# Performance work log

Measured on AMD Instinct MI355X. Metric: run time of the kernel, lower is better.

Reference implementation:

```python
import jax, jax.numpy as jnp
import numpy as np

BN_EPS = 1e-5


def _lin(x, W, b):
    return x @ W.T + b


def reference(input, first_skeleton, noise, first_W, first_b, gru_Wih, gru_Whh,
              gru_bih, gru_bhh, l0_W, l0_b, res_W, res_b, bn_g, bn_b, bn_m, bn_v,
              fl1_W, fl1_b, fl2_W, fl2_b, fl3_W, fl3_b, qkv_W,
              posm_W1, posm_b1, posm_W2, posm_b2, attn_W1, attn_b1, attn_W2, attn_b2):
    B = input.shape[0]
    # first skeleton embedding -> (B, 50, 1)
    sk = _lin(first_skeleton.reshape(B, 36), first_W, first_b).reshape(B, 50, 1)
    # GRU(10 -> 10), batch_first, h0 = 0
    def gru_step(h, x_t):
        gi = x_t @ gru_Wih.T + gru_bih          # (B, 30)
        gh = h @ gru_Whh.T + gru_bhh
        ir, iz, i_n = jnp.split(gi, 3, axis=-1)
        hr, hz, h_n = jnp.split(gh, 3, axis=-1)
        r = jax.nn.sigmoid(ir + hr)
        z = jax.nn.sigmoid(iz + hz)
        n = jnp.tanh(i_n + r * h_n)
        h_new = (1.0 - z) * n + z * h
        return h_new, h_new
    h0 = jnp.zeros((B, 10), input.dtype)
    _, aux = jax.lax.scan(gru_step, h0, jnp.swapaxes(noise, 0, 1))  # (50, B, 10)
    aux = jnp.tanh(jnp.swapaxes(aux, 0, 1))                          # (B, 50, 10)
    x = jnp.concatenate([input, aux, sk], axis=2).reshape(-1, 267)   # (B*50, 267)
    out = _lin(x, l0_W, l0_b)                                        # (B*50, 1024)
    # three residual Linear+BN(eval)+ReLU blocks
    for i in range(3):
        y = out
        for j in range(2):
            y = _lin(y, res_W[i, j], res_b[i, j])
            y = bn_g[i, j] * (y - bn_m[i, j]) * jax.lax.rsqrt(bn_v[i, j] + BN_EPS) + bn_b[i, j]
            y = jax.nn.relu(y)
        out = y + out
    # dropout: eval mode (identity)
    feats = _lin(out, fl1_W, fl1_b).reshape(B, 50, 128)
    pos = _lin(out, fl2_W, fl2_b).reshape(B, 50, 3)
    # PointTransformerLayer (full attention, mask all True -> no-op)
    qkv = feats @ qkv_W.T                                   # (B, 50, 384)
    q, k, v = jnp.split(qkv, 3, axis=-1)
    rel_pos = pos[:, :, None, :] - pos[:, None, :, :]        # (B, 50, 50, 3)
    rel_emb = _lin(jax.nn.relu(_lin(rel_pos, posm_W1, posm_b1)), posm_W2, posm_b2)  # (B,50,50,128)
    qk_rel = q[:, :, None, :] - k[:, None, :, :]             # (B, 50, 50, 128)
    v_ij = v[:, None, :, :] + rel_emb                        # (B, 50, 50, 128)
    sim = _lin(jax.nn.relu(_lin(qk_rel + rel_emb, attn_W1, attn_b1)), attn_W2, attn_b2)
    attn = jax.nn.softmax(sim, axis=-2)                      # softmax over j
    agg = jnp.einsum('bijd,bijd->bid', attn, v_ij)           # (B, 50, 128)
    o = jnp.tanh(_lin(agg, fl3_W, fl3_b))                    # (B, 50, 36)
    return o


def setup_inputs() -> dict:
    key = jax.random.key(0)
    ks = iter(jax.random.split(key, 64))
    def W(*s):
        return jax.random.normal(next(ks), s, jnp.float32) * 0.02
    B = 256
    z = lambda *s: jnp.zeros(s, jnp.float32)
    return {
        'input': jax.random.normal(next(ks), (B, 50, 256), jnp.float32),
        'first_skeleton': jax.random.normal(next(ks), (B, 36), jnp.float32),
        'noise': jax.random.normal(next(ks), (B, 50, 10), jnp.float32) * 0.33,
        'first_W': W(50, 36), 'first_b': z(50),
        'gru_Wih': W(30, 10), 'gru_Whh': W(30, 10), 'gru_bih': z(30), 'gru_bhh': z(30),
        'l0_W': W(1024, 267), 'l0_b': z(1024),
        'res_W': W(3, 2, 1024, 1024), 'res_b': z(3, 2, 1024),
        'bn_g': jnp.ones((3, 2, 1024), jnp.float32), 'bn_b': z(3, 2, 1024),
        'bn_m': z(3, 2, 1024), 'bn_v': jnp.ones((3, 2, 1024), jnp.float32),
        'fl1_W': W(128, 1024), 'fl1_b': z(128),
        'fl2_W': W(3, 1024), 'fl2_b': z(3),
        'fl3_W': W(36, 128), 'fl3_b': z(36),
        'qkv_W': W(384, 128),
        'posm_W1': W(64, 3), 'posm_b1': z(64), 'posm_W2': W(128, 64), 'posm_b2': z(128),
        'attn_W1': W(512, 128), 'attn_b1': z(512), 'attn_W2': W(128, 512), 'attn_b2': z(128),
    }
```

## Files before the change

kernel.cpp:

```cpp
#include <hip/hip_runtime.h>

typedef __attribute__((ext_vector_type(8))) short bf16x8;
typedef __attribute__((ext_vector_type(4))) float f32x4;
typedef __attribute__((ext_vector_type(4))) ushort u16x4;

__device__ __forceinline__ unsigned f2b2(float lo, float hi) {
    unsigned r;
    asm("v_cvt_pk_bf16_f32 %0, %1, %2" : "=v"(r) : "v"(lo), "v"(hi));
    return r;
}
__device__ __forceinline__ ushort f2b(float v) {
    return (ushort)f2b2(v, v);
}
__device__ __forceinline__ float b2f(ushort b) {
    union { float f; unsigned u; } x; x.u = ((unsigned)b) << 16; return x.f;
}

__device__ __forceinline__ void gl_lds16(const void* g, void* l) {
    __builtin_amdgcn_global_load_lds(
        (__attribute__((address_space(1))) void*)(g),
        (__attribute__((address_space(3))) void*)(l), 16, 0, 0);
}


__global__ void k_split(const float* __restrict__ src, ushort* __restrict__ hi,
                        ushort* __restrict__ lo, int rows, int K, int Kpad) {
    long total = (long)rows * Kpad;
    for (long idx = (long)blockIdx.x * 256 + threadIdx.x; idx < total;
         idx += (long)gridDim.x * 256) {
        int r = (int)(idx / Kpad), c = (int)(idx % Kpad);
        float v = (c < K) ? src[(long)r * K + c] : 0.f;
        ushort h = f2b(v);
        hi[idx] = h;
        if (lo) lo[idx] = f2b(v - b2f(h));
    }
}

__global__ void k_wc(const float* __restrict__ qkvW, const float* __restrict__ fl1W,
                     const float* __restrict__ fl1b, float* __restrict__ Wc,
                     float* __restrict__ bc) {
    int idx = blockIdx.x * 256 + threadIdx.x;
    if (idx >= 384 * 1024) return;
    int n = idx >> 10, k = idx & 1023;
    float s = 0.f;
    #pragma unroll 8
    for (int d = 0; d < 128; ++d) s += qkvW[n * 128 + d] * fl1W[d * 1024 + k];
    Wc[idx] = s;
    if (k == 0) {
        float sb = 0.f;
        #pragma unroll 8
        for (int d = 0; d < 128; ++d) sb += qkvW[n * 128 + d] * fl1b[d];
        bc[n] = sb;
    }
}

__global__ void k_sk(const float* __restrict__ fs, const float* __restrict__ fW,
                     const float* __restrict__ fb, float* __restrict__ sk) {
    int m = blockIdx.x * 256 + threadIdx.x;
    if (m >= 12800) return;
    int b = m / 50, i = m % 50;
    float s = fb[i];
    #pragma unroll 4
    for (int c = 0; c < 36; ++c) s += fs[b * 36 + c] * fW[i * 36 + c];
    sk[m] = s;
}

__global__ void k_gru(const float* __restrict__ noise, const float* __restrict__ Wih,
                      const float* __restrict__ Whh, const float* __restrict__ bih,
                      const float* __restrict__ bhh, float* __restrict__ aux) {
    int lane = threadIdx.x & 63;
    int b = blockIdx.x;
    if (b >= 256) return;
    float wih[10] = {}, whh[10] = {};
    float bi = 0.f, bh = 0.f;
    if (lane < 30) {
        #pragma unroll
        for (int c = 0; c < 10; ++c) { wih[c] = Wih[lane * 10 + c]; whh[c] = Whh[lane * 10 + c]; }
        bi = bih[lane]; bh = bhh[lane];
    }
    float h = 0.f;
    for (int t = 0; t < 50; ++t) {
        float xr = (lane < 10) ? noise[(b * 50 + t) * 10 + lane] : 0.f;
        float gi = bi, gh = bh;
        #pragma unroll
        for (int c = 0; c < 10; ++c) {
            float xc = __shfl(xr, c, 64);
            float hc = __shfl(h, c, 64);
            gi += wih[c] * xc; gh += whh[c] * hc;
        }
        float siz = __shfl(gi, lane + 10, 64), shz = __shfl(gh, lane + 10, 64);
        float sin_ = __shfl(gi, lane + 20, 64), shn = __shfl(gh, lane + 20, 64);
        float r = 1.f / (1.f + expf(-(gi + gh)));
        float z = 1.f / (1.f + expf(-(siz + shz)));
        float n = tanhf(sin_ + r * shn);
        float hn = (1.f - z) * n + z * h;
        if (lane < 10) { h = hn; aux[(b * 50 + t) * 10 + lane] = tanhf(hn); }
    }
}

__global__ void k_xbuild(const float* __restrict__ input, const float* __restrict__ aux,
                         const float* __restrict__ sk, ushort* __restrict__ xhi,
                         long M) {
    long idx = (long)blockIdx.x * 256 + threadIdx.x;
    if (idx >= M * 288) return;
    int m = (int)(idx / 288), c = (int)(idx % 288);
    float v;
    if (c < 256) v = input[(long)m * 256 + c];
    else if (c < 266) v = aux[m * 10 + (c - 256)];
    else if (c == 266) v = sk[m];
    else v = 0.f;
    xhi[idx] = f2b(v);
}

template <int MODE>
__global__ __launch_bounds__(256, 3) void k_gemm(
    const ushort* __restrict__ Ahi,
    const ushort* __restrict__ Bhi,
    int N, int K,
    float* outF, ushort* outHi,
    const float* __restrict__ bias,
    const float* __restrict__ bng, const float* __restrict__ bnb,
    const float* __restrict__ bnm, const float* __restrict__ bnv,
    const ushort* resHi) {
    __shared__ __align__(16) ushort S[2][128][32];
    int t = threadIdx.x;
    int flat = blockIdx.y * gridDim.x + blockIdx.x;
    int nwg = gridDim.x * gridDim.y;
    int q = nwg >> 3, r = nwg & 7;
    int xcd = flat & 7, seq = flat >> 3;
    int wgid = (xcd < r ? xcd * (q + 1) : r * (q + 1) + (xcd - r) * q) + seq;
    int bx = wgid % gridDim.x, by = wgid / gridDim.x;
    int m0 = by * 128, n0 = bx * 128;
    int w = t >> 6, lane = t & 63;
    int wm = w >> 1, wn = w & 1;
    int lo16 = lane & 15, hi4 = lane >> 4;

    const int srow = lane >> 2;
    const int skoff = ((lane & 3) ^ (srow & 3)) * 8;
    const int slot8 = (hi4 ^ (lo16 & 3)) * 8;

    f32x4 acc[4][4];
    #pragma unroll
    for (int i = 0; i < 4; ++i)
        #pragma unroll
        for (int j = 0; j < 4; ++j) acc[i][j] = f32x4{0.f, 0.f, 0.f, 0.f};

    const int nk = K / 32;
    for (int kt = 0; kt < nk; ++kt) {
        const int kb = kt * 32;
        #pragma unroll
        for (int i = 0; i < 2; ++i) {
            int rg = w * 32 + i * 16;
            long ga = (long)(m0 + rg + srow) * K + kb + skoff;
            long gb = (long)(n0 + rg + srow) * K + kb + skoff;
            gl_lds16(&Ahi[ga], &S[0][rg][0]);
            gl_lds16(&Bhi[gb], &S[1][rg][0]);
        }
        __syncthreads();
        bf16x8 ah[4], bh[4];
        #pragma unroll
        for (int m = 0; m < 4; ++m) {
            int row = wm * 64 + m * 16 + lo16;
            ah[m] = *(const bf16x8*)&S[0][row][slot8];
        }
        #pragma unroll
        for (int n = 0; n < 4; ++n) {
            int col = wn * 64 + n * 16 + lo16;
            bh[n] = *(const bf16x8*)&S[1][col][slot8];
        }
        #pragma unroll
        for (int m = 0; m < 4; ++m)
            #pragma unroll
            for (int n = 0; n < 4; ++n)
                acc[m][n] = __builtin_amdgcn_mfma_f32_16x16x32_bf16(ah[m], bh[n], acc[m][n], 0, 0, 0);
        __syncthreads();
    }

    #pragma unroll
    for (int n = 0; n < 4; ++n) {
        int gn = n0 + wn * 64 + n * 16 + lo16;
        float bv = bias ? bias[gn] : 0.f;
        float sc = 1.f, sh = 0.f;
        if (MODE >= 1) { sc = bng[gn] * rsqrtf(bnv[gn] + 1e-5f); sh = bnb[gn] - bnm[gn] * sc; }
        #pragma unroll
        for (int m = 0; m < 4; ++m)
            #pragma unroll
            for (int r2 = 0; r2 < 4; ++r2) {
                int gm = m0 + wm * 64 + m * 16 + hi4 * 4 + r2;
                long o = (long)gm * N + gn;
                float v = acc[m][n][r2] + bv;
                if (MODE >= 1) v = fmaxf(v * sc + sh, 0.f);
                if (MODE == 2) v += b2f(resHi[o]);
                if (outF) outF[o] = v;
                if (outHi) outHi[o] = f2b(v);
            }
    }
}

__global__ void k_fl2(const ushort* __restrict__ hA,
                      const float* __restrict__ W, const float* __restrict__ bias,
                      float* __restrict__ pos) {
    int w = threadIdx.x >> 6, lane = threadIdx.x & 63;
    int m = blockIdx.x * 4 + w;
    float a0 = 0.f, a1 = 0.f, a2 = 0.f;
    for (int k0 = lane * 4; k0 < 1024; k0 += 256) {
        long o = (long)m * 1024 + k0;
        u16x4 hv = *(const u16x4*)&hA[o];
        f32x4 w0 = *(const f32x4*)&W[k0];
        f32x4 w1 = *(const f32x4*)&W[1024 + k0];
        f32x4 w2 = *(const f32x4*)&W[2048 + k0];
        #pragma unroll
        for (int e = 0; e < 4; ++e) {
            float x = b2f(hv[e]);
            a0 += x * w0[e]; a1 += x * w1[e]; a2 += x * w2[e];
        }
    }
    #pragma unroll
    for (int off = 32; off; off >>= 1) {
        a0 += __shfl_xor(a0, off, 64);
        a1 += __shfl_xor(a1, off, 64);
        a2 += __shfl_xor(a2, off, 64);
    }
    if (lane == 0) {
        pos[m * 3 + 0] = a0 + bias[0];
        pos[m * 3 + 1] = a1 + bias[1];
        pos[m * 3 + 2] = a2 + bias[2];
    }
}

__global__ __launch_bounds__(256, 3) void k_sim(
    const float* __restrict__ qkv, const float* __restrict__ posb,
    const ushort* __restrict__ W1b, const ushort* __restrict__ W2b,
    const float* __restrict__ b1, const ushort* __restrict__ pW2b,
    const float* __restrict__ pW1, const float* __restrict__ pb1,
    const float* __restrict__ pb2, _Float16* __restrict__ sim) {
    __shared__ __align__(16) char smem[49152];
    int flat = blockIdx.x;
    int nwg = gridDim.x;
    int q = nwg >> 3, r = nwg & 7;
    int xcd = flat & 7, seq = flat >> 3;
    int wgid = (xcd < r ? xcd * (q + 1) : r * (q + 1) + (xcd - r) * q) + seq;
    int R0 = wgid * 128;
    int t = threadIdx.x, w = t >> 6, lane = t & 63;
    int lo16 = lane & 15, hi4 = lane >> 4;
    char* H1 = smem + 32768;

    {
        int rl = t & 127, eh = t >> 7;
        int g = R0 + rl;
        int bi = g / 50, j = g - bi * 50;
        int b = bi / 50;
        int kv = b * 50 + j;
        float d0 = posb[bi * 3] - posb[kv * 3];
        float d1 = posb[bi * 3 + 1] - posb[kv * 3 + 1];
        float d2 = posb[bi * 3 + 2] - posb[kv * 3 + 2];
        int swm = (rl & 7) << 4;
        #pragma unroll
        for (int e0 = 0; e0 < 32; e0 += 2) {
            int e = eh * 32 + e0;
            float v0 = fmaxf(pb1[e] + pW1[e * 3] * d0 + pW1[e * 3 + 1] * d1
                             + pW1[e * 3 + 2] * d2, 0.f);
            float v1 = fmaxf(pb1[e + 1] + pW1[e * 3 + 3] * d0 + pW1[e * 3 + 4] * d1
                             + pW1[e * 3 + 5] * d2, 0.f);
            *(unsigned*)(H1 + rl * 128 + ((e * 2) ^ swm)) = f2b2(v0, v1);
        }
    }
    __syncthreads();

    {
        f32x4 racc[8][2];
        #pragma unroll
        for (int m = 0; m < 8; ++m)
            #pragma unroll
            for (int n = 0; n < 2; ++n) racc[m][n] = f32x4{0.f, 0.f, 0.f, 0.f};
        #pragma unroll
        for (int kt = 0; kt < 2; ++kt) {
            int k0 = kt * 32 + hi4 * 8;
            bf16x8 bv[2];
            #pragma unroll
            for (int n = 0; n < 2; ++n)
                bv[n] = *(const bf16x8*)&pW2b[(w * 32 + n * 16 + lo16) * 64 + k0];
            #pragma unroll
            for (int m = 0; m < 8; ++m) {
                int row = m * 16 + lo16;
                bf16x8 ha = *(const bf16x8*)(H1 + row * 128 + ((k0 * 2) ^ ((lo16 & 7) << 4)));
                #pragma unroll
                for (int n = 0; n < 2; ++n)
                    racc[m][n] = __builtin_amdgcn_mfma_f32_16x16x32_bf16(ha, bv[n], racc[m][n], 0, 0, 0);
            }
        }
        #pragma unroll
        for (int m = 0; m < 8; ++m)
            #pragma unroll
            for (int n = 0; n < 2; ++n) {
                int col = w * 32 + n * 16 + lo16;
                float pb = pb2[col];
                #pragma unroll
                for (int rr = 0; rr < 4; ++rr) {
                    int row = m * 16 + hi4 * 4 + rr;
                    *(ushort*)(smem + row * 256 + ((col * 2) ^ ((row & 15) << 4))) =
                        f2b(racc[m][n][rr] + pb);
                }
            }
    }
    __syncthreads();

    #pragma unroll
    for (int cc = 0; cc < 8; ++cc) {
        int c = cc * 256 + t;
        int row = c >> 4, g16 = c & 15;
        int g = R0 + row;
        int bi = g / 50, j = g - bi * 50;
        int b = bi / 50;
        long kq = (long)bi * 384 + g16 * 8;
        long kk = (long)(b * 50 + j) * 384 + 128 + g16 * 8;
        f32x4 q0 = *(const f32x4*)&qkv[kq];
        f32x4 q1 = *(const f32x4*)&qkv[kq + 4];
        f32x4 k0v = *(const f32x4*)&qkv[kk];
        f32x4 k1v = *(const f32x4*)&qkv[kk + 4];
        char* addr = smem + row * 256 + ((g16 * 16) ^ ((row & 15) << 4));
        bf16x8 rv = *(bf16x8*)addr;
        bf16x8 tv;
        unsigned* tu = (unsigned*)&tv;
        #pragma unroll
        for (int i = 0; i < 2; ++i)
            tu[i] = f2b2(q0[2 * i] - k0v[2 * i] + b2f((ushort)rv[2 * i]),
                         q0[2 * i + 1] - k0v[2 * i + 1] + b2f((ushort)rv[2 * i + 1]));
        #pragma unroll
        for (int i = 0; i < 2; ++i)
            tu[2 + i] = f2b2(q1[2 * i] - k1v[2 * i] + b2f((ushort)rv[4 + 2 * i]),
                             q1[2 * i + 1] - k1v[2 * i + 1] + b2f((ushort)rv[4 + 2 * i + 1]));
        *(bf16x8*)addr = tv;
    }
    __syncthreads();

    f32x4 acc2[8][2];
    #pragma unroll
    for (int m = 0; m < 8; ++m)
        #pragma unroll
        for (int n = 0; n < 2; ++n) acc2[m][n] = f32x4{0.f, 0.f, 0.f, 0.f};

    for (int e8 = 0; e8 < 8; ++e8) {
        f32x4 acc1[8];
        #pragma unroll
        for (int m = 0; m < 8; ++m) acc1[m] = f32x4{0.f, 0.f, 0.f, 0.f};
        __builtin_amdgcn_s_setprio(1);
        #pragma unroll
        for (int kt = 0; kt < 4; ++kt) {
            int col = e8 * 64 + w * 16 + lo16;
            int k0 = kt * 32 + hi4 * 8;
            bf16x8 bfv = *(const bf16x8*)&W1b[(long)col * 128 + k0];
            #pragma unroll
            for (int m = 0; m < 8; ++m) {
                int row = m * 16 + lo16;
                bf16x8 af = *(const bf16x8*)(smem + row * 256 +
                              ((k0 * 2) ^ ((row & 15) << 4)));
                acc1[m] = __builtin_amdgcn_mfma_f32_16x16x32_bf16(af, bfv, acc1[m], 0, 0, 0);
            }
        }
        __builtin_amdgcn_s_setprio(0);
        __syncthreads();
        {
            int ch = w * 16 + lo16;
            float bb = b1[e8 * 64 + ch];
            #pragma unroll
            for (int m = 0; m < 8; ++m) {
                unsigned p01 = f2b2(fmaxf(acc1[m][0] + bb, 0.f), fmaxf(acc1[m][1] + bb, 0.f));
                unsigned p23 = f2b2(fmaxf(acc1[m][2] + bb, 0.f), fmaxf(acc1[m][3] + bb, 0.f));
                int r0 = m * 16 + hi4 * 4;
                *(ushort*)(H1 + (r0 + 0) * 128 + ((ch * 2) ^ (((r0 + 0) & 7) << 4))) = (ushort)p01;
                *(ushort*)(H1 + (r0 + 1) * 128 + ((ch * 2) ^ (((r0 + 1) & 7) << 4))) = (ushort)(p01 >> 16);
                *(ushort*)(H1 + (r0 + 2) * 128 + ((ch * 2) ^ (((r0 + 2) & 7) << 4))) = (ushort)p23;
                *(ushort*)(H1 + (r0 + 3) * 128 + ((ch * 2) ^ (((r0 + 3) & 7) << 4))) = (ushort)(p23 >> 16);
            }
        }
        __syncthreads();
        #pragma unroll
        for (int kt2 = 0; kt2 < 2; ++kt2) {
            int k0 = kt2 * 32 + hi4 * 8;
            bf16x8 af2[8];
            #pragma unroll
            for (int m = 0; m < 8; ++m) {
                int row = m * 16 + lo16;
                af2[m] = *(const bf16x8*)(H1 + row * 128 + ((k0 * 2) ^ ((lo16 & 7) << 4)));
            }
            __builtin_amdgcn_s_setprio(1);
            #pragma unroll
            for (int n = 0; n < 2; ++n) {
                int col = w * 32 + n * 16 + lo16;
                bf16x8 w2 = *(const bf16x8*)&W2b[(long)col * 512 + e8 * 64 + k0];
                #pragma unroll
                for (int m = 0; m < 8; ++m)
                    acc2[m][n] = __builtin_amdgcn_mfma_f32_16x16x32_bf16(af2[m], w2, acc2[m][n], 0, 0, 0);
            }
            __builtin_amdgcn_s_setprio(0);
        }
    }

    #pragma unroll
    for (int m = 0; m < 8; ++m)
        #pragma unroll
        for (int n = 0; n < 2; ++n) {
            int col = w * 32 + n * 16 + lo16;
            #pragma unroll
            for (int rr = 0; rr < 4; ++rr) {
                int row = m * 16 + hi4 * 4 + rr;
                sim[(long)(R0 + row) * 128 + col] = (_Float16)acc2[m][n][rr];
            }
        }
}

__global__ __launch_bounds__(256, 3) void k_soft(
    const float* __restrict__ qkv, const float* __restrict__ posb,
    const ushort* __restrict__ pW2b,
    const float* __restrict__ pW1, const float* __restrict__ pb1,
    const float* __restrict__ pb2, const _Float16* __restrict__ sim,
    const float* __restrict__ fl3W, const float* __restrict__ fl3b,
    float* __restrict__ out, long mbase) {
    __shared__ __align__(16) char smem[17472];
    int cpx = gridDim.x >> 3;
    int biL = (blockIdx.x & 7) * cpx + (blockIdx.x >> 3);
    int bL = biL / 50;
    int t = threadIdx.x, w = t >> 6, lane = t & 63;
    int lo16 = lane & 15, hi4 = lane >> 4;

    bf16x8 h_a[2];
    {
        const int jrow = w * 16 + lo16;
        const bool jvalid = jrow < 50;
        float pi0 = posb[biL * 3], pi1 = posb[biL * 3 + 1], pi2 = posb[biL * 3 + 2];
        float d0 = 0.f, d1 = 0.f, d2 = 0.f;
        if (jvalid) {
            int pj = (bL * 50 + jrow) * 3;
            d0 = pi0 - posb[pj]; d1 = pi1 - posb[pj + 1]; d2 = pi2 - posb[pj + 2];
        }
        #pragma unroll
        for (int kt = 0; kt < 2; ++kt) {
            float hv[8];
            #pragma unroll
            for (int e = 0; e < 8; ++e) {
                int ke = kt * 32 + hi4 * 8 + e;
                hv[e] = jvalid
                    ? fmaxf(pb1[ke] + pW1[ke * 3] * d0 + pW1[ke * 3 + 1] * d1
                            + pW1[ke * 3 + 2] * d2, 0.f)
                    : 0.f;
            }
            unsigned* hu = (unsigned*)&h_a[kt];
            #pragma unroll
            for (int i = 0; i < 4; ++i) hu[i] = f2b2(hv[2 * i], hv[2 * i + 1]);
        }
    }

    {
        f32x4 racc[8];
        #pragma unroll
        for (int n = 0; n < 8; ++n) racc[n] = f32x4{0.f, 0.f, 0.f, 0.f};
        #pragma unroll
        for (int kt = 0; kt < 2; ++kt) {
            int k0 = kt * 32 + hi4 * 8;
            #pragma unroll
            for (int n = 0; n < 8; ++n) {
                bf16x8 bv = *(const bf16x8*)&pW2b[(n * 16 + lo16) * 64 + k0];
                racc[n] = __builtin_amdgcn_mfma_f32_16x16x32_bf16(h_a[kt], bv, racc[n], 0, 0, 0);
            }
        }
        int j0 = w * 16 + hi4 * 4;
        #pragma unroll
        for (int n = 0; n < 8; ++n) {
            int col = n * 16 + lo16;
            float pb = pb2[col];
            unsigned p01 = f2b2(racc[n][0] + pb, racc[n][1] + pb);
            unsigned p23 = f2b2(racc[n][2] + pb, racc[n][3] + pb);
            *(ushort*)(smem + (j0 + 0) * 256 + ((col * 2) ^ (((j0 + 0) & 15) << 4))) = (ushort)p01;
            *(ushort*)(smem + (j0 + 1) * 256 + ((col * 2) ^ (((j0 + 1) & 15) << 4))) = (ushort)(p01 >> 16);
            *(ushort*)(smem + (j0 + 2) * 256 + ((col * 2) ^ (((j0 + 2) & 15) << 4))) = (ushort)p23;
            *(ushort*)(smem + (j0 + 3) * 256 + ((col * 2) ^ (((j0 + 3) & 15) << 4))) = (ushort)(p23 >> 16);
        }
    }
    __syncthreads();

    f32x4 acc2[4][2];
    #pragma unroll
    for (int m = 0; m < 4; ++m)
        #pragma unroll
        for (int n = 0; n < 2; ++n) {
            int col = w * 32 + n * 16 + lo16;
            #pragma unroll
            for (int rr = 0; rr < 4; ++rr) {
                int j = m * 16 + hi4 * 4 + rr;
                acc2[m][n][rr] = (j < 50)
                    ? (float)sim[(long)(biL * 50 + j) * 128 + col] : 0.f;
            }
        }

    float outv[2];
    #pragma unroll
    for (int n = 0; n < 2; ++n) {
        float mx = -1e30f;
        #pragma unroll
        for (int m = 0; m < 4; ++m)
            #pragma unroll
            for (int rr = 0; rr < 4; ++rr) {
                int j = m * 16 + hi4 * 4 + rr;
                if (j < 50) mx = fmaxf(mx, acc2[m][n][rr]);
            }
        mx = fmaxf(mx, __shfl_xor(mx, 16, 64));
        mx = fmaxf(mx, __shfl_xor(mx, 32, 64));
        float e[4][4];
        float sum = 0.f;
        #pragma unroll
        for (int m = 0; m < 4; ++m)
            #pragma unroll
            for (int rr = 0; rr < 4; ++rr) {
                int j = m * 16 + hi4 * 4 + rr;
                float ev = (j < 50) ? __expf(acc2[m][n][rr] - mx) : 0.f;
                e[m][rr] = ev; sum += ev;
            }
        sum += __shfl_xor(sum, 16, 64);
        sum += __shfl_xor(sum, 32, 64);
        float inv = 1.f / sum;
        int col = w * 32 + n * 16 + lo16;
        float ag = 0.f;
        #pragma unroll
        for (int m = 0; m < 4; ++m)
            #pragma unroll
            for (int rr = 0; rr < 4; ++rr) {
                int j = m * 16 + hi4 * 4 + rr;
                if (j < 50) {
                    float rl = b2f(*(const ushort*)(smem + j * 256 +
                                  ((col * 2) ^ ((j & 15) << 4))));
                    float vv = qkv[(long)(bL * 50 + j) * 384 + 256 + col] + rl;
                    ag += e[m][rr] * inv * vv;
                }
            }
        ag += __shfl_xor(ag, 16, 64);
        ag += __shfl_xor(ag, 32, 64);
        outv[n] = ag;
    }
    float* aggF = (float*)(smem + 16384);
    float* part = (float*)(smem + 16896);
    if (hi4 == 0) {
        aggF[w * 32 + lo16] = outv[0];
        aggF[w * 32 + 16 + lo16] = outv[1];
    }
    if (lane < 36) {
        const float* wf = &fl3W[lane * 128 + w * 32];
        const float* af = aggF + w * 32;
        float s = 0.f;
        #pragma unroll 8
        for (int d = 0; d < 32; ++d) s += af[d] * wf[d];
        part[w * 36 + lane] = s;
    }
    __syncthreads();

    if (t < 36) {
        float s = fl3b[t] + part[t] + part[36 + t] + part[72 + t] + part[108 + t];
        out[(mbase + biL) * 36 + t] = tanhf(s);
    }
}

struct Bufs {
    float *sk, *aux, *qkvF, *posb, *WcF, *bc;
    ushort *xh, *actAh, *actBh;
    ushort *l0Wh, *resWh, *Wch, *aW1b, *aW2b, *pW2b;
    ushort *sim;
};

static size_t plan_ws(char* ws, long MCr, Bufs& B) {
    size_t off = 0;
    auto alloc = [&](size_t n) { char* p = ws + off; off += (n + 255) & ~(size_t)255; return p; };
    B.sk    = (float*) alloc(12800L * 4);
    B.aux   = (float*) alloc(128000L * 4);
    B.xh    = (ushort*)alloc((size_t)MCr * 288 * 2);
    B.actAh = (ushort*)alloc((size_t)MCr * 1024 * 2);
    B.actBh = (ushort*)alloc((size_t)MCr * 1024 * 2);
    B.qkvF  = (float*) alloc((size_t)MCr * 384 * 4);
    B.posb  = (float*) alloc((size_t)MCr * 3 * 4);
    B.sim   = (ushort*)alloc((size_t)MCr * 50 * 128 * 2);
    B.l0Wh  = (ushort*)alloc(1024L * 288 * 2);
    B.resWh = (ushort*)alloc(6144L * 1024 * 2);
    B.WcF   = (float*) alloc(384L * 1024 * 4);
    B.Wch   = (ushort*)alloc(384L * 1024 * 2);
    B.bc    = (float*) alloc(384L * 4);
    B.aW1b  = (ushort*)alloc(512L * 128 * 2);
    B.aW2b  = (ushort*)alloc(128L * 512 * 2);
    B.pW2b  = (ushort*)alloc(128L * 64 * 2);
    return off;
}

extern "C" void kernel_launch(void* const* d_in, const int* in_sizes, int n_in,
                              void* d_out, int out_size, void* d_ws, size_t ws_size,
                              hipStream_t stream) {
    (void)in_sizes; (void)n_in;
    const float* input  = (const float*)d_in[0];
    const float* fskel  = (const float*)d_in[1];
    const float* noise  = (const float*)d_in[2];
    const float* firstW = (const float*)d_in[3];
    const float* firstB = (const float*)d_in[4];
    const float* gWih   = (const float*)d_in[5];
    const float* gWhh   = (const float*)d_in[6];
    const float* gbih   = (const float*)d_in[7];
    const float* gbhh   = (const float*)d_in[8];
    const float* l0W    = (const float*)d_in[9];
    const float* l0b    = (const float*)d_in[10];
    const float* resW   = (const float*)d_in[11];
    const float* resB   = (const float*)d_in[12];
    const float* bnG    = (const float*)d_in[13];
    const float* bnB    = (const float*)d_in[14];
    const float* bnM    = (const float*)d_in[15];
    const float* bnV    = (const float*)d_in[16];
    const float* fl1W   = (const float*)d_in[17];
    const float* fl1b   = (const float*)d_in[18];
    const float* fl2W   = (const float*)d_in[19];
    const float* fl2b   = (const float*)d_in[20];
    const float* fl3W   = (const float*)d_in[21];
    const float* fl3b   = (const float*)d_in[22];
    const float* qkvW   = (const float*)d_in[23];
    const float* pW1    = (const float*)d_in[24];
    const float* pb1    = (const float*)d_in[25];
    const float* pW2    = (const float*)d_in[26];
    const float* pb2    = (const float*)d_in[27];
    const float* aW1    = (const float*)d_in[28];
    const float* ab1    = (const float*)d_in[29];
    const float* aW2    = (const float*)d_in[30];
    float* out = (float*)d_out;

    char* ws = (char*)d_ws;
    Bufs B;
    long MCr = 12800;
    while (plan_ws(ws, MCr, B) > ws_size) {
        MCr >>= 1;
        if (MCr < 1600) {
            hipMemsetAsync(d_out, 0, (size_t)out_size * sizeof(float), stream);
            return;
        }
    }
    const int nchunks = (int)(12800 / MCr);

    k_split<<<1152, 256, 0, stream>>>(l0W, B.l0Wh, nullptr, 1024, 267, 288);
    k_split<<<8192, 256, 0, stream>>>(resW, B.resWh, nullptr, 6144, 1024, 1024);
    k_wc<<<1536, 256, 0, stream>>>(qkvW, fl1W, fl1b, B.WcF, B.bc);
    k_split<<<1536, 256, 0, stream>>>(B.WcF, B.Wch, nullptr, 384, 1024, 1024);
    k_split<<<256, 256, 0, stream>>>(aW1, B.aW1b, nullptr, 512, 128, 128);
    k_split<<<256, 256, 0, stream>>>(aW2, B.aW2b, nullptr, 128, 512, 512);
    k_split<<<32, 256, 0, stream>>>(pW2, B.pW2b, nullptr, 128, 64, 64);
    k_sk<<<50, 256, 0, stream>>>(fskel, firstW, firstB, B.sk);
    k_gru<<<256, 64, 0, stream>>>(noise, gWih, gWhh, gbih, gbhh, B.aux);

    for (int c = 0; c < nchunks; ++c) {
        long mbase = (long)c * MCr;
        int xb_grid = (int)((MCr * 288 + 255) / 256);
        k_xbuild<<<xb_grid, 256, 0, stream>>>(input + mbase * 256, B.aux + mbase * 10,
                                              B.sk + mbase, B.xh, MCr);
        dim3 gt(8, (unsigned)(MCr / 128));
        k_gemm<0><<<gt, 256, 0, stream>>>(B.xh, B.l0Wh, 1024, 288,
            nullptr, B.actAh, l0b, nullptr, nullptr, nullptr, nullptr, nullptr);
        for (int blk = 0; blk < 3; ++blk) {
            int j0 = blk * 2, j1 = blk * 2 + 1;
            k_gemm<1><<<gt, 256, 0, stream>>>(B.actAh,
                B.resWh + (size_t)j0 * 1024 * 1024,
                1024, 1024, nullptr, B.actBh, resB + j0 * 1024,
                bnG + j0 * 1024, bnB + j0 * 1024, bnM + j0 * 1024, bnV + j0 * 1024,
                nullptr);
            k_gemm<2><<<gt, 256, 0, stream>>>(B.actBh,
                B.resWh + (size_t)j1 * 1024 * 1024,
                1024, 1024, nullptr, B.actAh, resB + j1 * 1024,
                bnG + j1 * 1024, bnB + j1 * 1024, bnM + j1 * 1024, bnV + j1 * 1024,
                B.actAh);
        }
        dim3 gq(3, (unsigned)(MCr / 128));
        k_gemm<0><<<gq, 256, 0, stream>>>(B.actAh, B.Wch, 384, 1024,
            B.qkvF, nullptr, B.bc, nullptr, nullptr, nullptr, nullptr, nullptr);
        k_fl2<<<(int)(MCr / 4), 256, 0, stream>>>(B.actAh, fl2W, fl2b, B.posb);
        int nsim = (int)(MCr * 50 / 128);
        k_sim<<<nsim, 256, 0, stream>>>(B.qkvF, B.posb, B.aW1b, B.aW2b, ab1, B.pW2b,
                                        pW1, pb1, pb2, (_Float16*)B.sim);
        k_soft<<<(int)MCr, 256, 0, stream>>>(B.qkvF, B.posb, B.pW2b, pW1, pb1, pb2,
                                             (const _Float16*)B.sim, fl3W, fl3b,
                                             out, mbase);
    }
}
```

Baseline: 942.1 us.

## Fuse similarity MLP and softmax aggregation into one attention kernel

```diff
diff --git a/kernel.cpp b/kernel.cpp
--- a/kernel.cpp
+++ b/kernel.cpp
@@ -228,32 +228,33 @@
     }
 }
 
-__global__ __launch_bounds__(256, 3) void k_sim(
+__global__ __launch_bounds__(256, 3) void k_attn2(
     const float* __restrict__ qkv, const float* __restrict__ posb,
     const ushort* __restrict__ W1b, const ushort* __restrict__ W2b,
     const float* __restrict__ b1, const ushort* __restrict__ pW2b,
     const float* __restrict__ pW1, const float* __restrict__ pb1,
-    const float* __restrict__ pb2, _Float16* __restrict__ sim) {
+    const float* __restrict__ pb2,
+    const float* __restrict__ fl3W, const float* __restrict__ fl3b,
+    float* __restrict__ out, long mbase) {
     __shared__ __align__(16) char smem[49152];
-    int flat = blockIdx.x;
-    int nwg = gridDim.x;
+    int flat = blockIdx.x, nwg = gridDim.x;
     int q = nwg >> 3, r = nwg & 7;
     int xcd = flat & 7, seq = flat >> 3;
     int wgid = (xcd < r ? xcd * (q + 1) : r * (q + 1) + (xcd - r) * q) + seq;
-    int R0 = wgid * 128;
+    int bi0 = wgid * 2;
     int t = threadIdx.x, w = t >> 6, lane = t & 63;
     int lo16 = lane & 15, hi4 = lane >> 4;
     char* H1 = smem + 32768;
 
     {
         int rl = t & 127, eh = t >> 7;
-        int g = R0 + rl;
-        int bi = g / 50, j = g - bi * 50;
-        int b = bi / 50;
-        int kv = b * 50 + j;
-        float d0 = posb[bi * 3] - posb[kv * 3];
-        float d1 = posb[bi * 3 + 1] - posb[kv * 3 + 1];
-        float d2 = posb[bi * 3 + 2] - posb[kv * 3 + 2];
+        int biL = bi0 + (rl >> 6);
+        int j = rl & 63; int jc = j < 50 ? j : 49;
+        int bL = biL / 50;
+        int kv = bL * 50 + jc;
+        float d0 = posb[biL * 3] - posb[kv * 3];
+        float d1 = posb[biL * 3 + 1] - posb[kv * 3 + 1];
+        float d2 = posb[biL * 3 + 2] - posb[kv * 3 + 2];
         int swm = (rl & 7) << 4;
         #pragma unroll
         for (int e0 = 0; e0 < 32; e0 += 2) {
@@ -309,27 +310,32 @@
     for (int cc = 0; cc < 8; ++cc) {
         int c = cc * 256 + t;
         int row = c >> 4, g16 = c & 15;
-        int g = R0 + row;
-        int bi = g / 50, j = g - bi * 50;
-        int b = bi / 50;
-        long kq = (long)bi * 384 + g16 * 8;
-        long kk = (long)(b * 50 + j) * 384 + 128 + g16 * 8;
-        f32x4 q0 = *(const f32x4*)&qkv[kq];
-        f32x4 q1 = *(const f32x4*)&qkv[kq + 4];
-        f32x4 k0v = *(const f32x4*)&qkv[kk];
-        f32x4 k1v = *(const f32x4*)&qkv[kk + 4];
+        int biL = bi0 + (row >> 6);
+        int j = row & 63;
         char* addr = smem + row * 256 + ((g16 * 16) ^ ((row & 15) << 4));
-        bf16x8 rv = *(bf16x8*)addr;
         bf16x8 tv;
-        unsigned* tu = (unsigned*)&tv;
-        #pragma unroll
-        for (int i = 0; i < 2; ++i)
-            tu[i] = f2b2(q0[2 * i] - k0v[2 * i] + b2f((ushort)rv[2 * i]),
-                         q0[2 * i + 1] - k0v[2 * i + 1] + b2f((ushort)rv[2 * i + 1]));
-        #pragma unroll
-        for (int i = 0; i < 2; ++i)
-            tu[2 + i] = f2b2(q1[2 * i] - k1v[2 * i] + b2f((ushort)rv[4 + 2 * i]),
-                             q1[2 * i + 1] - k1v[2 * i + 1] + b2f((ushort)rv[4 + 2 * i + 1]));
+        if (j < 50) {
+            int bL = biL / 50;
+            long kq = (long)biL * 384 + g16 * 8;
+            long kk = (long)(bL * 50 + j) * 384 + 128 + g16 * 8;
+            f32x4 q0 = *(const f32x4*)&qkv[kq];
+            f32x4 q1 = *(const f32x4*)&qkv[kq + 4];
+            f32x4 k0v = *(const f32x4*)&qkv[kk];
+            f32x4 k1v = *(const f32x4*)&qkv[kk + 4];
+            bf16x8 rv = *(bf16x8*)addr;
+            unsigned* tu = (unsigned*)&tv;
+            #pragma unroll
+            for (int i = 0; i < 2; ++i)
+                tu[i] = f2b2(q0[2 * i] - k0v[2 * i] + b2f((ushort)rv[2 * i]),
+                             q0[2 * i + 1] - k0v[2 * i + 1] + b2f((ushort)rv[2 * i + 1]));
+            #pragma unroll
+            for (int i = 0; i < 2; ++i)
+                tu[2 + i] = f2b2(q1[2 * i] - k1v[2 * i] + b2f((ushort)rv[4 + 2 * i]),
+                                 q1[2 * i + 1] - k1v[2 * i + 1] + b2f((ushort)rv[4 + 2 * i + 1]));
+        } else {
+            #pragma unroll
+            for (int e = 0; e < 8; ++e) tv[e] = 0;
+        }
         *(bf16x8*)addr = tv;
     }
     __syncthreads();
@@ -396,166 +402,142 @@
             __builtin_amdgcn_s_setprio(0);
         }
     }
-
-    #pragma unroll
-    for (int m = 0; m < 8; ++m)
-        #pragma unroll
-        for (int n = 0; n < 2; ++n) {
-            int col = w * 32 + n * 16 + lo16;
-            #pragma unroll
-            for (int rr = 0; rr < 4; ++rr) {
-                int row = m * 16 + hi4 * 4 + rr;
-                sim[(long)(R0 + row) * 128 + col] = (_Float16)acc2[m][n][rr];
-            }
-        }
-}
-
-__global__ __launch_bounds__(256, 3) void k_soft(
-    const float* __restrict__ qkv, const float* __restrict__ posb,
-    const ushort* __restrict__ pW2b,
-    const float* __restrict__ pW1, const float* __restrict__ pb1,
-    const float* __restrict__ pb2, const _Float16* __restrict__ sim,
-    const float* __restrict__ fl3W, const float* __restrict__ fl3b,
-    float* __restrict__ out, long mbase) {
-    __shared__ __align__(16) char smem[17472];
-    int cpx = gridDim.x >> 3;
-    int biL = (blockIdx.x & 7) * cpx + (blockIdx.x >> 3);
-    int bL = biL / 50;
-    int t = threadIdx.x, w = t >> 6, lane = t & 63;
-    int lo16 = lane & 15, hi4 = lane >> 4;
-
-    bf16x8 h_a[2];
+    __syncthreads();
+
     {
-        const int jrow = w * 16 + lo16;
-        const bool jvalid = jrow < 50;
-        float pi0 = posb[biL * 3], pi1 = posb[biL * 3 + 1], pi2 = posb[biL * 3 + 2];
-        float d0 = 0.f, d1 = 0.f, d2 = 0.f;
-        if (jvalid) {
-            int pj = (bL * 50 + jrow) * 3;
-            d0 = pi0 - posb[pj]; d1 = pi1 - posb[pj + 1]; d2 = pi2 - posb[pj + 2];
-        }
-        #pragma unroll
-        for (int kt = 0; kt < 2; ++kt) {
-            float hv[8];
-            #pragma unroll
-            for (int e = 0; e < 8; ++e) {
-                int ke = kt * 32 + hi4 * 8 + e;
-                hv[e] = jvalid
-                    ? fmaxf(pb1[ke] + pW1[ke * 3] * d0 + pW1[ke * 3 + 1] * d1
-                            + pW1[ke * 3 + 2] * d2, 0.f)
-                    : 0.f;
-            }
-            unsigned* hu = (unsigned*)&h_a[kt];
-            #pragma unroll
-            for (int i = 0; i < 4; ++i) hu[i] = f2b2(hv[2 * i], hv[2 * i + 1]);
-        }
-    }
+        int rl = t & 127, eh = t >> 7;
+        int biL = bi0 + (rl >> 6);
+        int j = rl & 63; int jc = j < 50 ? j : 49;
+        int bL = biL / 50;
+        int kv = bL * 50 + jc;
+        float d0 = posb[biL * 3] - posb[kv * 3];
+        float d1 = posb[biL * 3 + 1] - posb[kv * 3 + 1];
+        float d2 = posb[biL * 3 + 2] - posb[kv * 3 + 2];
+        int swm = (rl & 7) << 4;
+        #pragma unroll
+        for (int e0 = 0; e0 < 32; e0 += 2) {
+            int e = eh * 32 + e0;
+            float v0 = fmaxf(pb1[e] + pW1[e * 3] * d0 + pW1[e * 3 + 1] * d1
+                             + pW1[e * 3 + 2] * d2, 0.f);
+            float v1 = fmaxf(pb1[e + 1] + pW1[e * 3 + 3] * d0 + pW1[e * 3 + 4] * d1
+                             + pW1[e * 3 + 5] * d2, 0.f);
+            *(unsigned*)(H1 + rl * 128 + ((e * 2) ^ swm)) = f2b2(v0, v1);
+        }
+    }
+    __syncthreads();
 
     {
-        f32x4 racc[8];
-        #pragma unroll
-        for (int n = 0; n < 8; ++n) racc[n] = f32x4{0.f, 0.f, 0.f, 0.f};
+        f32x4 racc[8][2];
+        #pragma unroll
+        for (int m = 0; m < 8; ++m)
+            #pragma unroll
+            for (int n = 0; n < 2; ++n) racc[m][n] = f32x4{0.f, 0.f, 0.f, 0.f};
         #pragma unroll
         for (int kt = 0; kt < 2; ++kt) {
             int k0 = kt * 32 + hi4 * 8;
-            #pragma unroll
-            for (int n = 0; n < 8; ++n) {
-                bf16x8 bv = *(const bf16x8*)&pW2b[(n * 16 + lo16) * 64 + k0];
-                racc[n] = __builtin_amdgcn_mfma_f32_16x16x32_bf16(h_a[kt], bv, racc[n], 0, 0, 0);
-            }
-        }
-        int j0 = w * 16 + hi4 * 4;
-        #pragma unroll
-        for (int n = 0; n < 8; ++n) {
-            int col = n * 16 + lo16;
-            float pb = pb2[col];
-            unsigned p01 = f2b2(racc[n][0] + pb, racc[n][1] + pb);
-            unsigned p23 = f2b2(racc[n][2] + pb, racc[n][3] + pb);
-            *(ushort*)(smem + (j0 + 0) * 256 + ((col * 2) ^ (((j0 + 0) & 15) << 4))) = (ushort)p01;
-            *(ushort*)(smem + (j0 + 1) * 256 + ((col * 2) ^ (((j0 + 1) & 15) << 4))) = (ushort)(p01 >> 16);
-            *(ushort*)(smem + (j0 + 2) * 256 + ((col * 2) ^ (((j0 + 2) & 15) << 4))) = (ushort)p23;
-            *(ushort*)(smem + (j0 + 3) * 256 + ((col * 2) ^ (((j0 + 3) & 15) << 4))) = (ushort)(p23 >> 16);
-        }
+            bf16x8 bv[2];
+            #pragma unroll
+            for (int n = 0; n < 2; ++n)
+                bv[n] = *(const bf16x8*)&pW2b[(w * 32 + n * 16 + lo16) * 64 + k0];
+            #pragma unroll
+            for (int m = 0; m < 8; ++m) {
+                int row = m * 16 + lo16;
+                bf16x8 ha = *(const bf16x8*)(H1 + row * 128 + ((k0 * 2) ^ ((lo16 & 7) << 4)));
+                #pragma unroll
+                for (int n = 0; n < 2; ++n)
+                    racc[m][n] = __builtin_amdgcn_mfma_f32_16x16x32_bf16(ha, bv[n], racc[m][n], 0, 0, 0);
+            }
+        }
+        #pragma unroll
+        for (int m = 0; m < 8; ++m)
+            #pragma unroll
+            for (int n = 0; n < 2; ++n) {
+                int col = w * 32 + n * 16 + lo16;
+                float pb = pb2[col];
+                #pragma unroll
+                for (int rr = 0; rr < 4; ++rr) {
+                    int row = m * 16 + hi4 * 4 + rr;
+                    *(ushort*)(smem + row * 256 + ((col * 2) ^ ((row & 15) << 4))) =
+                        f2b(racc[m][n][rr] + pb);
+                }
+            }
     }
     __syncthreads();
 
-    f32x4 acc2[4][2];
+    float* aggF = (float*)H1;
+    float* part = (float*)(H1 + 1024);
     #pragma unroll
-    for (int m = 0; m < 4; ++m)
+    for (int bs = 0; bs < 2; ++bs) {
+        int biL = bi0 + bs;
+        int bL = biL / 50;
+        float outv[2];
         #pragma unroll
         for (int n = 0; n < 2; ++n) {
+            float mx = -1e30f;
+            #pragma unroll
+            for (int m = 0; m < 4; ++m)
+                #pragma unroll
+                for (int rr = 0; rr < 4; ++rr) {
+                    int j = m * 16 + hi4 * 4 + rr;
+                    if (j < 50) mx = fmaxf(mx, acc2[bs * 4 + m][n][rr]);
+                }
+            mx = fmaxf(mx, __shfl_xor(mx, 16, 64));
+            mx = fmaxf(mx, __shfl_xor(mx, 32, 64));
+            float e[4][4];
+            float sum = 0.f;
+            #pragma unroll
+            for (int m = 0; m < 4; ++m)
+                #pragma unroll
+                for (int rr = 0; rr < 4; ++rr) {
+                    int j = m * 16 + hi4 * 4 + rr;
+                    float ev = (j < 50) ? __expf(acc2[bs * 4 + m][n][rr] - mx) : 0.f;
+                    e[m][rr] = ev; sum += ev;
+                }
+            sum += __shfl_xor(sum, 16, 64);
+            sum += __shfl_xor(sum, 32, 64);
+            float inv = 1.f / sum;
             int col = w * 32 + n * 16 + lo16;
-            #pragma unroll
-            for (int rr = 0; rr < 4; ++rr) {
-                int j = m * 16 + hi4 * 4 + rr;
-                acc2[m][n][rr] = (j < 50)
-                    ? (float)sim[(long)(biL * 50 + j) * 128 + col] : 0.f;
-            }
-        }
-
-    float outv[2];
-    #pragma unroll
-    for (int n = 0; n < 2; ++n) {
-        float mx = -1e30f;
-        #pragma unroll
-        for (int m = 0; m < 4; ++m)
-            #pragma unroll
-            for (int rr = 0; rr < 4; ++rr) {
-                int j = m * 16 + hi4 * 4 + rr;
-                if (j < 50) mx = fmaxf(mx, acc2[m][n][rr]);
-            }
-        mx = fmaxf(mx, __shfl_xor(mx, 16, 64));
-        mx = fmaxf(mx, __shfl_xor(mx, 32, 64));
-        float e[4][4];
-        float sum = 0.f;
-        #pragma unroll
-        for (int m = 0; m < 4; ++m)
-            #pragma unroll
-            for (int rr = 0; rr < 4; ++rr) {
-                int j = m * 16 + hi4 * 4 + rr;
-                float ev = (j < 50) ? __expf(acc2[m][n][rr] - mx) : 0.f;
-                e[m][rr] = ev; sum += ev;
-            }
-        sum += __shfl_xor(sum, 16, 64);
-        sum += __shfl_xor(sum, 32, 64);
-        float inv = 1.f / sum;
-        int col = w * 32 + n * 16 + lo16;
-        float ag = 0.f;
-        #pragma unroll
-        for (int m = 0; m < 4; ++m)
-            #pragma unroll
-            for (int rr = 0; rr < 4; ++rr) {
-                int j = m * 16 + hi4 * 4 + rr;
-                if (j < 50) {
-                    float rl = b2f(*(const ushort*)(smem + j * 256 +
-                                  ((col * 2) ^ ((j & 15) << 4))));
-                    float vv = qkv[(long)(bL * 50 + j) * 384 + 256 + col] + rl;
-                    ag += e[m][rr] * inv * vv;
+            float ag = 0.f;
+            #pragma unroll
+            for (int m = 0; m < 4; ++m)
+                #pragma unroll
+                for (int rr = 0; rr < 4; ++rr) {
+                    int j = m * 16 + hi4 * 4 + rr;
+                    if (j < 50) {
+                        int row = bs * 64 + j;
+                        float rl = b2f(*(const ushort*)(smem + row * 256 +
+                                      ((col * 2) ^ ((j & 15) << 4))));
+                        float vv = qkv[(long)(bL * 50 + j) * 384 + 256 + col] + rl;
+                        ag += e[m][rr] * inv * vv;
+                    }
                 }
-            }
-        ag += __shfl_xor(ag, 16, 64);
-        ag += __shfl_xor(ag, 32, 64);
-        outv[n] = ag;
-    }
-    float* aggF = (float*)(smem + 16384);
-    float* part = (float*)(smem + 16896);
-    if (hi4 == 0) {
-        aggF[w * 32 + lo16] = outv[0];
-        aggF[w * 32 + 16 + lo16] = outv[1];
-    }
-    if (lane < 36) {
-        const float* wf = &fl3W[lane * 128 + w * 32];
-        const float* af = aggF + w * 32;
-        float s = 0.f;
-        #pragma unroll 8
-        for (int d = 0; d < 32; ++d) s += af[d] * wf[d];
-        part[w * 36 + lane] = s;
+            ag += __shfl_xor(ag, 16, 64);
+            ag += __shfl_xor(ag, 32, 64);
+            outv[n] = ag;
+        }
+        if (hi4 == 0) {
+            aggF[bs * 128 + w * 32 + lo16] = outv[0];
+            aggF[bs * 128 + w * 32 + 16 + lo16] = outv[1];
+        }
+        if (lane < 36) {
+            const float* wf = &fl3W[lane * 128 + w * 32];
+            const float* af = aggF + bs * 128 + w * 32;
+            float s = 0.f;
+            #pragma unroll 8
+            for (int d = 0; d < 32; ++d) s += af[d] * wf[d];
+            part[bs * 144 + w * 36 + lane] = s;
+        }
     }
     __syncthreads();
 
     if (t < 36) {
         float s = fl3b[t] + part[t] + part[36 + t] + part[72 + t] + part[108 + t];
-        out[(mbase + biL) * 36 + t] = tanhf(s);
+        out[(mbase + bi0) * 36 + t] = tanhf(s);
+    } else if (t >= 128 && t < 164) {
+        int tt = t - 128;
+        float s = fl3b[tt] + part[144 + tt] + part[144 + 36 + tt]
+                + part[144 + 72 + tt] + part[144 + 108 + tt];
+        out[(mbase + bi0 + 1) * 36 + tt] = tanhf(s);
     }
 }
 
@@ -563,7 +545,6 @@
     float *sk, *aux, *qkvF, *posb, *WcF, *bc;
     ushort *xh, *actAh, *actBh;
     ushort *l0Wh, *resWh, *Wch, *aW1b, *aW2b, *pW2b;
-    ushort *sim;
 };
 
 static size_t plan_ws(char* ws, long MCr, Bufs& B) {
@@ -576,7 +557,6 @@
     B.actBh = (ushort*)alloc((size_t)MCr * 1024 * 2);
     B.qkvF  = (float*) alloc((size_t)MCr * 384 * 4);
     B.posb  = (float*) alloc((size_t)MCr * 3 * 4);
-    B.sim   = (ushort*)alloc((size_t)MCr * 50 * 128 * 2);
     B.l0Wh  = (ushort*)alloc(1024L * 288 * 2);
     B.resWh = (ushort*)alloc(6144L * 1024 * 2);
     B.WcF   = (float*) alloc(384L * 1024 * 4);
@@ -672,11 +652,8 @@
         k_gemm<0><<<gq, 256, 0, stream>>>(B.actAh, B.Wch, 384, 1024,
             B.qkvF, nullptr, B.bc, nullptr, nullptr, nullptr, nullptr, nullptr);
         k_fl2<<<(int)(MCr / 4), 256, 0, stream>>>(B.actAh, fl2W, fl2b, B.posb);
-        int nsim = (int)(MCr * 50 / 128);
-        k_sim<<<nsim, 256, 0, stream>>>(B.qkvF, B.posb, B.aW1b, B.aW2b, ab1, B.pW2b,
-                                        pW1, pb1, pb2, (_Float16*)B.sim);
-        k_soft<<<(int)MCr, 256, 0, stream>>>(B.qkvF, B.posb, B.pW2b, pW1, pb1, pb2,
-                                             (const _Float16*)B.sim, fl3W, fl3b,
-                                             out, mbase);
-    }
-}
+        k_attn2<<<(int)(MCr / 2), 256, 0, stream>>>(B.qkvF, B.posb, B.aW1b, B.aW2b,
+                                                    ab1, B.pW2b, pW1, pb1, pb2,
+                                                    fl3W, fl3b, out, mbase);
+    }
+}
```

Measured after the change: 1.139 ms. 1.21x slower.
